# Performance work log

Hardware: AMD Instinct MI355X
Metric: run time of the kernel (lower is better)

The kernel has to match this reference:

```python
import jax, jax.numpy as jnp
import numpy as np

N, E, D, G, L = 100000, 1600000, 64, 512, 3
EPS = 1e-5


def setup_inputs() -> dict:
    key = jax.random.key(0)
    ks = jax.random.split(key, 8)
    x = jax.random.normal(ks[0], (N, D), dtype=jnp.float32)
    edge_index = jax.random.randint(ks[1], (2, E), 0, N, dtype=jnp.int32)
    batch = jnp.sort(jax.random.randint(ks[2], (N,), 0, G, dtype=jnp.int32))
    s = 1.0 / np.sqrt(D)
    convW = jax.random.normal(ks[3], (L, D, D), dtype=jnp.float32) * s
    convB = jnp.zeros((L, D), jnp.float32)
    bn_g = jnp.ones((L, D), jnp.float32); bn_b = jnp.zeros((L, D), jnp.float32)
    ln_g = jnp.ones((L, D), jnp.float32); ln_b = jnp.zeros((L, D), jnp.float32)
    W1 = jax.random.normal(ks[4], (3 * D, 2 * D), dtype=jnp.float32) * (1.0 / np.sqrt(3 * D))
    b1 = jnp.zeros((2 * D,), jnp.float32)
    ln1_g = jnp.ones((2 * D,), jnp.float32); ln1_b = jnp.zeros((2 * D,), jnp.float32)
    W2 = jax.random.normal(ks[5], (2 * D, D), dtype=jnp.float32) * (1.0 / np.sqrt(2 * D))
    b2 = jnp.zeros((D,), jnp.float32)
    ln2_g = jnp.ones((D,), jnp.float32); ln2_b = jnp.zeros((D,), jnp.float32)
    W3 = jax.random.normal(ks[6], (D, 1), dtype=jnp.float32) * s
    b3 = jnp.zeros((1,), jnp.float32)
    return dict(x=x, edge_index=edge_index, batch=batch, convW=convW, convB=convB,
                bn_g=bn_g, bn_b=bn_b, ln_g=ln_g, ln_b=ln_b,
                W1=W1, b1=b1, ln1_g=ln1_g, ln1_b=ln1_b,
                W2=W2, b2=b2, ln2_g=ln2_g, ln2_b=ln2_b, W3=W3, b3=b3)


def _layer_norm(h, g, b):
    mu = jnp.mean(h, axis=-1, keepdims=True)
    var = jnp.mean((h - mu) ** 2, axis=-1, keepdims=True)
    return (h - mu) * jax.lax.rsqrt(var + EPS) * g + b


def _forward(x, edge_index, batch, convW, convB, bn_g, bn_b, ln_g, ln_b,
             W1, b1, ln1_g, ln1_b, W2, b2, ln2_g, ln2_b, W3, b3):
    n = x.shape[0]
    loops = jnp.arange(n, dtype=edge_index.dtype)
    src = jnp.concatenate([edge_index[0], loops])  # self-loops as in GCNConv
    dst = jnp.concatenate([edge_index[1], loops])
    deg = jax.ops.segment_sum(jnp.ones_like(src, dtype=x.dtype), dst, num_segments=n)
    dinv = jnp.where(deg > 0, jax.lax.rsqrt(deg), 0.0)
    norm = (dinv[src] * dinv[dst])[:, None]  # [E+N, 1]

    h = x
    for i in range(L):
        x_in = h
        hw = h @ convW[i]                                   # [N, D]
        agg = jax.ops.segment_sum(norm * hw[src], dst, num_segments=n) + convB[i]
        # BatchNorm1d (train-mode batch stats, biased var)
        mu = jnp.mean(agg, axis=0)
        var = jnp.mean((agg - mu) ** 2, axis=0)
        hb = (agg - mu) * jax.lax.rsqrt(var + EPS) * bn_g[i] + bn_b[i]
        if i > 0:
            hb = hb + x_in  # residual (shapes match: D == D)
        h = jax.nn.gelu(_layer_norm(hb, ln_g[i], ln_b[i]), approximate=False)

    # multi-pool over graphs
    cnt = jax.ops.segment_sum(jnp.ones((n,), x.dtype), batch, num_segments=G)[:, None]
    s = jax.ops.segment_sum(h, batch, num_segments=G)
    mean = s / jnp.maximum(cnt, 1.0)
    mx = jax.ops.segment_max(h, batch, num_segments=G)
    mx = jnp.where(cnt > 0, mx, 0.0)
    z = jnp.concatenate([mean, mx, s], axis=1)  # [G, 3D]

    z = jax.nn.gelu(_layer_norm(z @ W1 + b1, ln1_g, ln1_b), approximate=False)
    z = jax.nn.gelu(_layer_norm(z @ W2 + b2, ln2_g, ln2_b), approximate=False)
    return z @ W3 + b3  # [G, num_classes]


def reference(x, edge_index, batch, convW, convB, bn_g, bn_b, ln_g, ln_b,
              W1, b1, ln1_g, ln1_b, W2, b2, ln2_g, ln2_b, W3, b3):
    return _forward(x, edge_index, batch, convW, convB, bn_g, bn_b, ln_g, ln_b,
                    W1, b1, ln1_g, ln1_b, W2, b2, ln2_g, ln2_b, W3, b3)
```

## Files before the change

### kernel.cpp

```cpp
#include <hip/hip_runtime.h>
#include <hip/hip_bf16.h>
#include <hip/hip_fp16.h>

#define DD 64
#define EPSV 1e-5f
#define NSLICE 16

typedef __attribute__((ext_vector_type(4))) _Float16 f16x4;
typedef __attribute__((ext_vector_type(8))) _Float16 f16x8;
typedef __attribute__((ext_vector_type(4))) float f32x4;

static __device__ __forceinline__ float fatomic_add(float* p, float v) {
#if defined(__HIP_DEVICE_COMPILE__)
    return unsafeAtomicAdd(p, v);
#else
    return 0.f;
#endif
}

static __device__ __forceinline__ float gelu_exact(float x) {
    return 0.5f * x * (1.0f + erff(x * 0.70710678118654752f));
}

static __device__ __forceinline__ void acc_u4(float* a8, uint4 v) {
    const __half2* hp = reinterpret_cast<const __half2*>(&v);
#pragma unroll
    for (int p = 0; p < 4; ++p) {
        float2 f = __half22float2(hp[p]);
        a8[2 * p] += f.x;
        a8[2 * p + 1] += f.y;
    }
}

#define ACHUNK 2048
#define NBMAX 400

__global__ __launch_bounds__(1024) void k_bcount(const int* __restrict__ dst,
                                                 int* __restrict__ bucketCnt,
                                                 int e, int nbuck) {
    __shared__ int h[NBMAX];
    int t = threadIdx.x;
    for (int i = t; i < nbuck; i += 1024) h[i] = 0;
    __syncthreads();
    int base = blockIdx.x * 8192;
#pragma unroll
    for (int k = 0; k < 8; ++k) {
        int i = base + k * 1024 + t;
        if (i < e) atomicAdd(&h[dst[i] >> 8], 1);
    }
    __syncthreads();
    for (int i = t; i < nbuck; i += 1024)
        if (h[i]) atomicAdd(&bucketCnt[i], h[i]);
}

__global__ __launch_bounds__(512) void k_bscan2(const int* __restrict__ bucketCnt,
                                                int* __restrict__ bbase,
                                                int* __restrict__ bcur,
                                                int* __restrict__ offs,
                                                int nbuck, int etotal, int n) {
    __shared__ int ws[8];
    int t = threadIdx.x, lane = t & 63, wv = t >> 6;
    int v = (t < nbuck) ? bucketCnt[t] : 0;
    int x = v;
#pragma unroll
    for (int o = 1; o < 64; o <<= 1) {
        int u = __shfl_up(x, o, 64);
        if (lane >= o) x += u;
    }
    if (lane == 63) ws[wv] = x;
    __syncthreads();
    int add = 0;
    for (int w = 0; w < wv; ++w) add += ws[w];
    int excl = add + x - v;
    if (t < nbuck) {
        bbase[t] = excl;
        bcur[t] = excl;
    }
    if (t == 0) {
        bbase[nbuck] = etotal;
        offs[n] = etotal;
    }
}

__global__ __launch_bounds__(1024) void k_dhist(const int* __restrict__ off,
                                                int* __restrict__ dcount, int n) {
    __shared__ int h[256];
    int t = threadIdx.x;
    if (t < 256) h[t] = 0;
    __syncthreads();
    int i = blockIdx.x * 1024 + t;
    if (i < n) {
        int d = min(off[i + 1] - off[i], 255);
        atomicAdd(&h[d], 1);
    }
    __syncthreads();
    if (t < 256 && h[t]) atomicAdd(&dcount[t], h[t]);
}

__global__ __launch_bounds__(256) void k_dscan(const int* __restrict__ dcount,
                                               int* __restrict__ dcur) {
    __shared__ int ws[4];
    int t = threadIdx.x;
    int lane = t & 63, wv = t >> 6;
    int v = dcount[t];
    int x = v;
#pragma unroll
    for (int o = 1; o < 64; o <<= 1) {
        int u = __shfl_up(x, o, 64);
        if (lane >= o) x += u;
    }
    if (lane == 63) ws[wv] = x;
    __syncthreads();
    int add = 0;
    for (int w = 0; w < wv; ++w) add += ws[w];
    dcur[t] = add + x - v;
}

__global__ __launch_bounds__(1024) void k_dscatter(const int* __restrict__ off,
                                                   int* __restrict__ dcur,
                                                   int* __restrict__ perm, int n) {
    __shared__ int lcnt[256], lbase[256];
    int t = threadIdx.x;
    if (t < 256) lcnt[t] = 0;
    __syncthreads();
    int i = blockIdx.x * 1024 + t;
    int d = 0, rank = 0;
    if (i < n) {
        d = min(off[i + 1] - off[i], 255);
        rank = atomicAdd(&lcnt[d], 1);
    }
    __syncthreads();
    if (t < 256 && lcnt[t]) lbase[t] = atomicAdd(&dcur[t], lcnt[t]);
    __syncthreads();
    if (i < n) perm[lbase[d] + rank] = i;
}

__global__ __launch_bounds__(256) void k_binA(const int* __restrict__ src,
                                              const int* __restrict__ dst,
                                              int* __restrict__ ebuf,
                                              int* __restrict__ bcur,
                                              int e, int nbuck) {
    __shared__ int cnt[NBMAX], startb[NBMAX], posb[NBMAX], gbase[NBMAX];
    __shared__ int stage[ACHUNK];
    __shared__ unsigned short stb[ACHUNK];
    int t = threadIdx.x;
    for (int cbase = blockIdx.x * ACHUNK; cbase < e; cbase += gridDim.x * ACHUNK) {
        int cval = min(ACHUNK, e - cbase);
        for (int i = t; i < nbuck; i += 256) { cnt[i] = 0; posb[i] = 0; }
        __syncthreads();
        int eb[8], es[8];
#pragma unroll
        for (int k = 0; k < 8; ++k) {
            int i = t + k * 256;
            if (i < cval) {
                int s = src[cbase + i];
                int d = dst[cbase + i];
                eb[k] = d >> 8;
                es[k] = s | ((d & 255) << 24);
                atomicAdd(&cnt[eb[k]], 1);
            } else eb[k] = -1;
        }
        __syncthreads();
        if (t == 0) {
            int r = 0;
            for (int b2 = 0; b2 < nbuck; ++b2) { startb[b2] = r; r += cnt[b2]; }
        }
        __syncthreads();
        for (int i = t; i < nbuck; i += 256)
            if (cnt[i] > 0) gbase[i] = atomicAdd(&bcur[i], cnt[i]);
#pragma unroll
        for (int k = 0; k < 8; ++k)
            if (eb[k] >= 0) {
                int idx = startb[eb[k]] + atomicAdd(&posb[eb[k]], 1);
                stage[idx] = es[k];
                stb[idx] = (unsigned short)eb[k];
            }
        __syncthreads();
        for (int i = t; i < cval; i += 256) {
            int b2 = stb[i];
            ebuf[gbase[b2] + (i - startb[b2])] = stage[i];
        }
        __syncthreads();
    }
}

__global__ __launch_bounds__(256) void k_binB(const int* __restrict__ ebuf,
                                              const int* __restrict__ bbase,
                                              int* __restrict__ offs,
                                              float* __restrict__ dinv,
                                              int* __restrict__ csr, int n) {
    __shared__ int cnt[256], cur[256], ws[4];
    int b = blockIdx.x;
    int base = b << 8;
    int nn = min(256, n - base);
    int t = threadIdx.x;
    int e0 = bbase[b], e1 = bbase[b + 1];
    cnt[t] = 0;
    __syncthreads();
    for (int i = e0 + t; i < e1; i += 256)
        atomicAdd(&cnt[((unsigned)ebuf[i]) >> 24], 1);
    __syncthreads();
    int v = cnt[t];
    int lane = t & 63, wv = t >> 6;
    int x = v;
#pragma unroll
    for (int o = 1; o < 64; o <<= 1) {
        int u = __shfl_up(x, o, 64);
        if (lane >= o) x += u;
    }
    if (lane == 63) ws[wv] = x;
    __syncthreads();
    int add = 0;
    for (int w = 0; w < wv; ++w) add += ws[w];
    int excl = add + x - v;
    if (t < nn) {
        offs[base + t] = e0 + excl;
        dinv[base + t] = rsqrtf((float)v + 1.0f);
    }
    cur[t] = e0 + excl;
    __syncthreads();
    for (int i = e0 + t; i < e1; i += 256) {
        int packed = ebuf[i];
        int dl = ((unsigned)packed) >> 24;
        int pos = atomicAdd(&cur[dl], 1);
        csr[pos] = packed & 0x00FFFFFF;
    }
}

__global__ void k_misc(const float* __restrict__ x, const float* __restrict__ dinv,
                       __half* __restrict__ mA, __half* __restrict__ mB, int n,
                       const int* __restrict__ batch, int* __restrict__ bnd, int g) {
    int i = blockIdx.x * 256 + threadIdx.x;
    int total = n * 64;
    if (i < total) {
        mA[i] = __float2half_rn(x[i] * dinv[i >> 6]);
    } else if (i < total + 64) {
        mA[i] = __float2half_rn(0.f);
        mB[i] = __float2half_rn(0.f);
    }
    if (i < n) {
        int b = batch[i];
        if (i == 0)
            for (int q = 0; q <= b; ++q) bnd[q] = 0;
        else {
            int pb = batch[i - 1];
            for (int q = pb + 1; q <= b; ++q) bnd[q] = i;
        }
        if (i == n - 1)
            for (int q = b + 1; q <= g; ++q) bnd[q] = n;
    }
}

__global__ __launch_bounds__(256, 4) void k_gather_gemm(const int* __restrict__ off,
                                                        const int* __restrict__ csr,
                                                        const float* __restrict__ dinv,
                                                        const __half* __restrict__ m16,
                                                        const float* __restrict__ W,
                                                        const float* __restrict__ convB,
                                                        const int* __restrict__ perm,
                                                        float* __restrict__ agg,
                                                        float* __restrict__ gstat,
                                                        int n, int nzero) {
    __shared__ float sred[128];
    const int t = threadIdx.x;
    const int lane = t & 63, wv = t >> 6;
    const int g = lane >> 4, ln = lane & 15;

    f16x8 bfr[2][4];
#pragma unroll
    for (int kt = 0; kt < 2; ++kt)
#pragma unroll
        for (int nt = 0; nt < 4; ++nt) {
            f16x8 h;
#pragma unroll
            for (int j = 0; j < 8; ++j)
                h[j] = (_Float16)W[(32 * kt + 8 * g + j) * 64 + 16 * nt + ln];
            bfr[kt][nt] = h;
        }

    if (t < 128) sred[t] = 0.f;
    __syncthreads();

    const int ntiles = (n + 15) >> 4;
    const int tile = blockIdx.x * 4 + wv;
    float s_acc[4] = {0.f, 0.f, 0.f, 0.f}, q_acc[4] = {0.f, 0.f, 0.f, 0.f};

    if (tile < ntiles) {
        const int slot = tile * 16 + ln;
        const bool valid = slot < n;
        const int node = valid ? perm[slot] : -1;
        const int row_self = valid ? node : nzero;
        int a = 0, deg = 0;
        float dd = 0.f;
        if (valid) {
            a = off[node];
            deg = off[node + 1] - a;
            dd = dinv[node];
        }
        int md = deg;
#pragma unroll
        for (int o = 1; o < 64; o <<= 1) md = max(md, __shfl_xor(md, o, 64));

        float acc[2][8];
#pragma unroll
        for (int kt = 0; kt < 2; ++kt)
#pragma unroll
            for (int j = 0; j < 8; ++j) acc[kt][j] = 0.f;

        const uint4* mrow4 = (const uint4*)m16;
        {
            const uint4* rp = mrow4 + ((size_t)row_self << 3) + g;
            uint4 v0 = rp[0], v1 = rp[4];
            acc_u4(acc[0], v0);
            acc_u4(acc[1], v1);
        }
        int ecur[4];
#pragma unroll
        for (int k = 0; k < 4; ++k) ecur[k] = (k < deg) ? csr[a + k] : nzero;
        for (int i = 0; i < md; i += 4) {
            int enx[4];
#pragma unroll
            for (int k = 0; k < 4; ++k) enx[k] = (i + 4 + k < deg) ? csr[a + i + 4 + k] : nzero;
            uint4 v[4][2];
#pragma unroll
            for (int r = 0; r < 4; ++r) {
                const uint4* rp = mrow4 + ((size_t)ecur[r] << 3) + g;
                v[r][0] = rp[0];
                v[r][1] = rp[4];
            }
#pragma unroll
            for (int r = 0; r < 4; ++r) {
                acc_u4(acc[0], v[r][0]);
                acc_u4(acc[1], v[r][1]);
            }
#pragma unroll
            for (int k = 0; k < 4; ++k) ecur[k] = enx[k];
        }

        f32x4 c[4];
#pragma unroll
        for (int nt = 0; nt < 4; ++nt) c[nt] = (f32x4){0.f, 0.f, 0.f, 0.f};
#pragma unroll
        for (int kt = 0; kt < 2; ++kt) {
            f16x8 ah, ar;
#pragma unroll
            for (int j = 0; j < 8; ++j) {
                float v = acc[kt][j] * dd;
                _Float16 h = (_Float16)v;
                ah[j] = h;
                ar[j] = (_Float16)(v - (float)h);
            }
#pragma unroll
            for (int nt = 0; nt < 4; ++nt) {
                c[nt] = __builtin_amdgcn_mfma_f32_16x16x32_f16(ah, bfr[kt][nt], c[nt], 0, 0, 0);
                c[nt] = __builtin_amdgcn_mfma_f32_16x16x32_f16(ar, bfr[kt][nt], c[nt], 0, 0, 0);
            }
        }

        int prow[4];
#pragma unroll
        for (int i = 0; i < 4; ++i) prow[i] = __shfl(node, 4 * g + i, 64);
        const float bias[4] = {convB[ln], convB[16 + ln], convB[32 + ln], convB[48 + ln]};
#pragma unroll
        for (int nt = 0; nt < 4; ++nt) {
#pragma unroll
            for (int i = 0; i < 4; ++i) {
                if (prow[i] >= 0) {
                    float v = c[nt][i] + bias[nt];
                    agg[(size_t)prow[i] * 64 + 16 * nt + ln] = v;
                    s_acc[nt] += v;
                    q_acc[nt] += v * v;
                }
            }
        }
#pragma unroll
        for (int nt = 0; nt < 4; ++nt) {
            s_acc[nt] += __shfl_xor(s_acc[nt], 16, 64);
            s_acc[nt] += __shfl_xor(s_acc[nt], 32, 64);
            q_acc[nt] += __shfl_xor(q_acc[nt], 16, 64);
            q_acc[nt] += __shfl_xor(q_acc[nt], 32, 64);
        }
        if (g == 0) {
#pragma unroll
            for (int nt = 0; nt < 4; ++nt) {
                atomicAdd(&sred[16 * nt + ln], s_acc[nt]);
                atomicAdd(&sred[64 + 16 * nt + ln], q_acc[nt]);
            }
        }
    }
    __syncthreads();
    if (t < 64) {
        float* gs = gstat + (blockIdx.x & (NSLICE - 1)) * 128;
        fatomic_add(&gs[t], sred[t]);
        fatomic_add(&gs[64 + t], sred[64 + t]);
    }
}

__global__ __launch_bounds__(256) void k_bn_ln_gelu(const float* __restrict__ agg,
                                                    const __half* __restrict__ m16res,
                                                    const float* __restrict__ gstat,
                                                    const float* __restrict__ dinv,
                                                    const float* __restrict__ bng,
                                                    const float* __restrict__ bnb,
                                                    const float* __restrict__ lng,
                                                    const float* __restrict__ lnb,
                                                    __half* __restrict__ m16out,
                                                    int n, int has_res, int scale_out) {
    int t = threadIdx.x;
    int lane = t & 63, wv = t >> 6;
    float fs = 0.f, fq = 0.f;
#pragma unroll
    for (int s = 0; s < NSLICE; ++s) {
        fs += gstat[s * 128 + lane];
        fq += gstat[s * 128 + 64 + lane];
    }
    float invN = 1.0f / (float)n;
    float mu_c = fs * invN;
    float var_c = fq * invN - mu_c * mu_c;
    float bscale = rsqrtf(var_c + EPSV) * bng[lane];
    float bshift = bnb[lane];
    float lg = lng[lane], lb = lnb[lane];
    for (int r = blockIdx.x * 4 + wv; r < n; r += gridDim.x * 4) {
        float dd = dinv[r];
        float x = agg[(size_t)r * 64 + lane];
        float hb = (x - mu_c) * bscale + bshift;
        if (has_res) hb += __half2float(m16res[(size_t)r * 64 + lane]) * (1.0f / dd);
        float ssum = hb;
#pragma unroll
        for (int off = 32; off; off >>= 1) ssum += __shfl_xor(ssum, off, 64);
        float rmu = ssum * (1.f / 64.f);
        float d = hb - rmu;
        float vs = d * d;
#pragma unroll
        for (int off = 32; off; off >>= 1) vs += __shfl_xor(vs, off, 64);
        float rvar = vs * (1.f / 64.f);
        float ln = d * rsqrtf(rvar + EPSV) * lg + lb;
        float g = gelu_exact(ln);
        float outv = scale_out ? g * dd : g;
        m16out[(size_t)r * 64 + lane] = __float2half_rn(outv);
    }
}

__global__ __launch_bounds__(256) void k_pool_z(const __half* __restrict__ h,
                                                const int* __restrict__ bnd,
                                                float* __restrict__ z) {
    int g = blockIdx.x;
    int t = threadIdx.x;
    int lane = t & 63, wv = t >> 6;
    int s0 = bnd[g], e0 = bnd[g + 1];
    float s = 0.f, mx = -INFINITY;
    for (int i = s0 + wv; i < e0; i += 4) {
        float v = __half2float(h[(size_t)i * 64 + lane]);
        s += v;
        mx = fmaxf(mx, v);
    }
    __shared__ float ss[256], sm[256];
    ss[t] = s;
    sm[t] = mx;
    __syncthreads();
    if (t < 64) {
        float fs = ss[t] + ss[t + 64] + ss[t + 128] + ss[t + 192];
        float fm = fmaxf(fmaxf(sm[t], sm[t + 64]), fmaxf(sm[t + 128], sm[t + 192]));
        float cntf = (float)(e0 - s0);
        float mean = fs / fmaxf(cntf, 1.0f);
        if (e0 == s0) fm = 0.f;
        z[g * 192 + t] = mean;
        z[g * 192 + 64 + t] = fm;
        z[g * 192 + 128 + t] = fs;
    }
}

__global__ __launch_bounds__(128) void k_head(const float* __restrict__ z,
                                              const float* __restrict__ W1, const float* __restrict__ b1,
                                              const float* __restrict__ ln1g, const float* __restrict__ ln1b,
                                              const float* __restrict__ W2, const float* __restrict__ b2,
                                              const float* __restrict__ ln2g, const float* __restrict__ ln2b,
                                              const float* __restrict__ W3, const float* __restrict__ b3,
                                              float* __restrict__ out) {
    int g = blockIdx.x;
    int t = threadIdx.x;
    int lane = t & 63, wv = t >> 6;
    __shared__ float zl[192], h1[128], red[2];
    for (int i = t; i < 192; i += 128) zl[i] = z[g * 192 + i];
    __syncthreads();
    float acc = b1[t];
    for (int k = 0; k < 192; ++k) acc += zl[k] * W1[k * 128 + t];
    float s = acc;
#pragma unroll
    for (int off = 32; off; off >>= 1) s += __shfl_xor(s, off, 64);
    if (lane == 0) red[wv] = s;
    __syncthreads();
    float mu = (red[0] + red[1]) * (1.f / 128.f);
    float d = acc - mu;
    float q = d * d;
#pragma unroll
    for (int off = 32; off; off >>= 1) q += __shfl_xor(q, off, 64);
    __syncthreads();
    if (lane == 0) red[wv] = q;
    __syncthreads();
    float var = (red[0] + red[1]) * (1.f / 128.f);
    float ln = d * rsqrtf(var + EPSV) * ln1g[t] + ln1b[t];
    h1[t] = gelu_exact(ln);
    __syncthreads();
    if (t < 64) {
        float acc2 = b2[t];
        for (int k = 0; k < 128; ++k) acc2 += h1[k] * W2[k * 64 + t];
        float s2 = acc2;
#pragma unroll
        for (int off = 32; off; off >>= 1) s2 += __shfl_xor(s2, off, 64);
        float mu2 = s2 * (1.f / 64.f);
        float d2 = acc2 - mu2;
        float q2 = d2 * d2;
#pragma unroll
        for (int off = 32; off; off >>= 1) q2 += __shfl_xor(q2, off, 64);
        float var2 = q2 * (1.f / 64.f);
        float l2 = d2 * rsqrtf(var2 + EPSV) * ln2g[t] + ln2b[t];
        float g2 = gelu_exact(l2);
        float p = g2 * W3[t];
#pragma unroll
        for (int off = 32; off; off >>= 1) p += __shfl_xor(p, off, 64);
        if (t == 0) out[g] = p + b3[0];
    }
}

extern "C" void kernel_launch(void* const* d_in, const int* in_sizes, int n_in,
                              void* d_out, int out_size, void* d_ws, size_t ws_size,
                              hipStream_t stream) {
    const float* x      = (const float*)d_in[0];
    const int*   eidx   = (const int*)d_in[1];
    const int*   batch  = (const int*)d_in[2];
    const float* convW  = (const float*)d_in[3];
    const float* convB  = (const float*)d_in[4];
    const float* bn_g   = (const float*)d_in[5];
    const float* bn_b   = (const float*)d_in[6];
    const float* ln_g   = (const float*)d_in[7];
    const float* ln_b   = (const float*)d_in[8];
    const float* W1     = (const float*)d_in[9];
    const float* b1     = (const float*)d_in[10];
    const float* ln1g   = (const float*)d_in[11];
    const float* ln1b   = (const float*)d_in[12];
    const float* W2     = (const float*)d_in[13];
    const float* b2     = (const float*)d_in[14];
    const float* ln2g   = (const float*)d_in[15];
    const float* ln2b   = (const float*)d_in[16];
    const float* W3     = (const float*)d_in[17];
    const float* b3     = (const float*)d_in[18];
    float* out = (float*)d_out;

    const int N = in_sizes[0] / DD;
    const int E = in_sizes[1] / 2;
    const int G = out_size;
    const int* esrc = eidx;
    const int* edst = eidx + E;

    char* ws = (char*)d_ws;
    size_t off_b = 0;
    auto alloc = [&](size_t bytes) {
        size_t p = off_b;
        off_b = (off_b + bytes + 255) & ~(size_t)255;
        return (void*)(ws + p);
    };
    int*    offs   = (int*)alloc((size_t)(N + 1) * 4);
    float*  dinv   = (float*)alloc((size_t)N * 4);
    int*    csr    = (int*)alloc((size_t)E * 4);
    int*    ebuf   = (int*)alloc((size_t)E * 4);
    __half* m16A   = (__half*)alloc((size_t)(N + 1) * DD * 2);
    __half* m16B   = (__half*)alloc((size_t)(N + 1) * DD * 2);
    float*  aggbuf = (float*)alloc((size_t)N * DD * 4);
    float*  gstats = (float*)alloc((size_t)3 * NSLICE * 128 * 4);
    int*    perm   = (int*)alloc((size_t)N * 4);
    int*    dcount = (int*)alloc(256 * 4);
    int*    dcur   = (int*)alloc(256 * 4);
    int*    bnd    = (int*)alloc((size_t)(G + 1) * 4);
    int*    bucketCnt = (int*)alloc((size_t)NBMAX * 4);
    int*    bbase  = (int*)alloc((size_t)(NBMAX + 1) * 4);
    int*    bcur   = (int*)alloc(((size_t)(N + 255) / 256) * 4);
    float* z = aggbuf;
    (void)ws_size; (void)n_in;

    const int nbuck = (N + 255) / 256;
    const int nb = (N + 1023) / 1024;

    hipMemsetAsync(gstats, 0, (size_t)3 * NSLICE * 128 * 4, stream);
    hipMemsetAsync(dcount, 0, 256 * 4, stream);
    hipMemsetAsync(bucketCnt, 0, (size_t)NBMAX * 4, stream);
    k_bcount<<<(E + 8191) / 8192, 1024, 0, stream>>>(edst, bucketCnt, E, nbuck);
    k_bscan2<<<1, 512, 0, stream>>>(bucketCnt, bbase, bcur, offs, nbuck, E, N);
    k_binA<<<(E + ACHUNK - 1) / ACHUNK, 256, 0, stream>>>(esrc, edst, ebuf, bcur, E, nbuck);
    k_binB<<<nbuck, 256, 0, stream>>>(ebuf, bbase, offs, dinv, csr, N);
    k_dhist<<<nb, 1024, 0, stream>>>(offs, dcount, N);
    k_dscan<<<1, 256, 0, stream>>>(dcount, dcur);
    k_dscatter<<<nb, 1024, 0, stream>>>(offs, dcur, perm, N);
    k_misc<<<((N + 1) * DD + 255) / 256, 256, 0, stream>>>(x, dinv, m16A, m16B, N, batch, bnd, G);

    __half* gin[3]  = {m16A, m16B, m16A};
    __half* gout[3] = {m16B, m16A, m16B};

    const int ntiles = (N + 15) / 16;
    const int gblocks = (ntiles + 3) / 4;

    for (int l = 0; l < 3; ++l) {
        float* gstat = gstats + (size_t)l * NSLICE * 128;
        k_gather_gemm<<<gblocks, 256, 0, stream>>>(offs, csr, dinv, (const __half*)gin[l],
                                                   convW + (size_t)l * DD * DD, convB + l * DD,
                                                   perm, aggbuf, gstat, N, N);
        k_bn_ln_gelu<<<2048, 256, 0, stream>>>(aggbuf, gin[l], gstat, dinv,
                                               bn_g + l * DD, bn_b + l * DD,
                                               ln_g + l * DD, ln_b + l * DD,
                                               gout[l], N, l > 0 ? 1 : 0, l < 2 ? 1 : 0);
    }

    k_pool_z<<<G, 256, 0, stream>>>(m16B, bnd, z);
    k_head<<<G, 128, 0, stream>>>(z, W1, b1, ln1g, ln1b, W2, b2, ln2g, ln2b, W3, b3, out);
}
```

Before: 418.6 us.

## Fuse prep kernels, precompute slot info, store aggregates in fp16, merge pool and head

Several independent changes. The x*dinv fp16 conversion moves into k_binB and the batch boundary setup into k_dhist, which removes k_misc. A k_slotinfo pass packs per-slot offset, degree, node and dinv into int4 so the gather kernel needs one load instead of chained perm/off/dinv loads. The aggregate buffer becomes fp16, halving its write and read traffic between the GEMM and BN kernels at some precision cost. Pooling and the MLP head are fused into one kernel, and the three memsets are merged into one.

```diff
diff --git a/kernel.cpp b/kernel.cpp
--- a/kernel.cpp
+++ b/kernel.cpp
@@ -83,7 +83,12 @@
 }
 
 __global__ __launch_bounds__(1024) void k_dhist(const int* __restrict__ off,
-                                                int* __restrict__ dcount, int n) {
+                                                int* __restrict__ dcount,
+                                                const int* __restrict__ batch,
+                                                int* __restrict__ bnd,
+                                                __half* __restrict__ mA,
+                                                __half* __restrict__ mB,
+                                                int n, int g) {
     __shared__ int h[256];
     int t = threadIdx.x;
     if (t < 256) h[t] = 0;
@@ -92,6 +97,19 @@
     if (i < n) {
         int d = min(off[i + 1] - off[i], 255);
         atomicAdd(&h[d], 1);
+        int b = batch[i];
+        if (i == 0)
+            for (int q = 0; q <= b; ++q) bnd[q] = 0;
+        else {
+            int pb = batch[i - 1];
+            for (int q = pb + 1; q <= b; ++q) bnd[q] = i;
+        }
+        if (i == n - 1)
+            for (int q = b + 1; q <= g; ++q) bnd[q] = n;
+    }
+    if (blockIdx.x == 0 && t < 64) {
+        mA[(size_t)n * 64 + t] = __float2half_rn(0.f);
+        mB[(size_t)n * 64 + t] = __float2half_rn(0.f);
     }
     __syncthreads();
     if (t < 256 && h[t]) atomicAdd(&dcount[t], h[t]);
@@ -133,6 +151,22 @@
     if (t < 256 && lcnt[t]) lbase[t] = atomicAdd(&dcur[t], lcnt[t]);
     __syncthreads();
     if (i < n) perm[lbase[d] + rank] = i;
+}
+
+__global__ __launch_bounds__(1024) void k_slotinfo(const int* __restrict__ off,
+                                                   const float* __restrict__ dinv,
+                                                   const int* __restrict__ perm,
+                                                   int4* __restrict__ sinfo,
+                                                   int n, int ntiles) {
+    int s = blockIdx.x * 1024 + threadIdx.x;
+    if (s < n) {
+        int node = perm[s];
+        int a = off[node];
+        int d = off[node + 1] - a;
+        sinfo[s] = make_int4(a, d, node, __float_as_int(dinv[node]));
+    } else if (s < ntiles * 16) {
+        sinfo[s] = make_int4(0, 0, -1, 0);
+    }
 }
 
 __global__ __launch_bounds__(256) void k_binA(const int* __restrict__ src,
@@ -186,10 +220,13 @@
 
 __global__ __launch_bounds__(256) void k_binB(const int* __restrict__ ebuf,
                                               const int* __restrict__ bbase,
+                                              const float* __restrict__ x,
                                               int* __restrict__ offs,
                                               float* __restrict__ dinv,
+                                              __half* __restrict__ mA,
                                               int* __restrict__ csr, int n) {
     __shared__ int cnt[256], cur[256], ws[4];
+    __shared__ float sdinv[256];
     int b = blockIdx.x;
     int base = b << 8;
     int nn = min(256, n - base);
@@ -202,23 +239,31 @@
     __syncthreads();
     int v = cnt[t];
     int lane = t & 63, wv = t >> 6;
-    int x = v;
+    int x2 = v;
 #pragma unroll
     for (int o = 1; o < 64; o <<= 1) {
-        int u = __shfl_up(x, o, 64);
-        if (lane >= o) x += u;
-    }
-    if (lane == 63) ws[wv] = x;
+        int u = __shfl_up(x2, o, 64);
+        if (lane >= o) x2 += u;
+    }
+    if (lane == 63) ws[wv] = x2;
     __syncthreads();
     int add = 0;
     for (int w = 0; w < wv; ++w) add += ws[w];
-    int excl = add + x - v;
+    int excl = add + x2 - v;
+    float dv = rsqrtf((float)v + 1.0f);
     if (t < nn) {
         offs[base + t] = e0 + excl;
-        dinv[base + t] = rsqrtf((float)v + 1.0f);
-    }
+        dinv[base + t] = dv;
+    }
+    sdinv[t] = dv;
     cur[t] = e0 + excl;
     __syncthreads();
+    const int tot = nn * 64;
+    const size_t gbase2 = (size_t)base * 64;
+    for (int i = t; i < tot; i += 256) {
+        float val = x[gbase2 + i] * sdinv[i >> 6];
+        mA[gbase2 + i] = __float2half_rn(val);
+    }
     for (int i = e0 + t; i < e1; i += 256) {
         int packed = ebuf[i];
         int dl = ((unsigned)packed) >> 24;
@@ -227,38 +272,12 @@
     }
 }
 
-__global__ void k_misc(const float* __restrict__ x, const float* __restrict__ dinv,
-                       __half* __restrict__ mA, __half* __restrict__ mB, int n,
-                       const int* __restrict__ batch, int* __restrict__ bnd, int g) {
-    int i = blockIdx.x * 256 + threadIdx.x;
-    int total = n * 64;
-    if (i < total) {
-        mA[i] = __float2half_rn(x[i] * dinv[i >> 6]);
-    } else if (i < total + 64) {
-        mA[i] = __float2half_rn(0.f);
-        mB[i] = __float2half_rn(0.f);
-    }
-    if (i < n) {
-        int b = batch[i];
-        if (i == 0)
-            for (int q = 0; q <= b; ++q) bnd[q] = 0;
-        else {
-            int pb = batch[i - 1];
-            for (int q = pb + 1; q <= b; ++q) bnd[q] = i;
-        }
-        if (i == n - 1)
-            for (int q = b + 1; q <= g; ++q) bnd[q] = n;
-    }
-}
-
-__global__ __launch_bounds__(256, 4) void k_gather_gemm(const int* __restrict__ off,
+__global__ __launch_bounds__(256, 4) void k_gather_gemm(const int4* __restrict__ sinfo,
                                                         const int* __restrict__ csr,
-                                                        const float* __restrict__ dinv,
                                                         const __half* __restrict__ m16,
                                                         const float* __restrict__ W,
                                                         const float* __restrict__ convB,
-                                                        const int* __restrict__ perm,
-                                                        float* __restrict__ agg,
+                                                        __half* __restrict__ agg,
                                                         float* __restrict__ gstat,
                                                         int n, int nzero) {
     __shared__ float sred[128];
@@ -277,6 +296,7 @@
                 h[j] = (_Float16)W[(32 * kt + 8 * g + j) * 64 + 16 * nt + ln];
             bfr[kt][nt] = h;
         }
+    const float bias[4] = {convB[ln], convB[16 + ln], convB[32 + ln], convB[48 + ln]};
 
     if (t < 128) sred[t] = 0.f;
     __syncthreads();
@@ -284,19 +304,14 @@
     const int ntiles = (n + 15) >> 4;
     const int tile = blockIdx.x * 4 + wv;
     float s_acc[4] = {0.f, 0.f, 0.f, 0.f}, q_acc[4] = {0.f, 0.f, 0.f, 0.f};
+    const uint4* mrow4 = (const uint4*)m16;
 
     if (tile < ntiles) {
-        const int slot = tile * 16 + ln;
-        const bool valid = slot < n;
-        const int node = valid ? perm[slot] : -1;
-        const int row_self = valid ? node : nzero;
-        int a = 0, deg = 0;
-        float dd = 0.f;
-        if (valid) {
-            a = off[node];
-            deg = off[node + 1] - a;
-            dd = dinv[node];
-        }
+        const int4 si = sinfo[tile * 16 + ln];
+        const int a = si.x, deg = si.y, node = si.z;
+        const float dd = __int_as_float(si.w);
+        const int row_self = (node >= 0) ? node : nzero;
+
         int md = deg;
 #pragma unroll
         for (int o = 1; o < 64; o <<= 1) md = max(md, __shfl_xor(md, o, 64));
@@ -307,7 +322,6 @@
 #pragma unroll
             for (int j = 0; j < 8; ++j) acc[kt][j] = 0.f;
 
-        const uint4* mrow4 = (const uint4*)m16;
         {
             const uint4* rp = mrow4 + ((size_t)row_self << 3) + g;
             uint4 v0 = rp[0], v1 = rp[4];
@@ -360,32 +374,32 @@
         int prow[4];
 #pragma unroll
         for (int i = 0; i < 4; ++i) prow[i] = __shfl(node, 4 * g + i, 64);
-        const float bias[4] = {convB[ln], convB[16 + ln], convB[32 + ln], convB[48 + ln]};
 #pragma unroll
         for (int nt = 0; nt < 4; ++nt) {
 #pragma unroll
             for (int i = 0; i < 4; ++i) {
                 if (prow[i] >= 0) {
                     float v = c[nt][i] + bias[nt];
-                    agg[(size_t)prow[i] * 64 + 16 * nt + ln] = v;
+                    agg[(size_t)prow[i] * 64 + 16 * nt + ln] = __float2half_rn(v);
                     s_acc[nt] += v;
                     q_acc[nt] += v * v;
                 }
             }
         }
+    }
+
+#pragma unroll
+    for (int nt = 0; nt < 4; ++nt) {
+        s_acc[nt] += __shfl_xor(s_acc[nt], 16, 64);
+        s_acc[nt] += __shfl_xor(s_acc[nt], 32, 64);
+        q_acc[nt] += __shfl_xor(q_acc[nt], 16, 64);
+        q_acc[nt] += __shfl_xor(q_acc[nt], 32, 64);
+    }
+    if (g == 0) {
 #pragma unroll
         for (int nt = 0; nt < 4; ++nt) {
-            s_acc[nt] += __shfl_xor(s_acc[nt], 16, 64);
-            s_acc[nt] += __shfl_xor(s_acc[nt], 32, 64);
-            q_acc[nt] += __shfl_xor(q_acc[nt], 16, 64);
-            q_acc[nt] += __shfl_xor(q_acc[nt], 32, 64);
-        }
-        if (g == 0) {
-#pragma unroll
-            for (int nt = 0; nt < 4; ++nt) {
-                atomicAdd(&sred[16 * nt + ln], s_acc[nt]);
-                atomicAdd(&sred[64 + 16 * nt + ln], q_acc[nt]);
-            }
+            atomicAdd(&sred[16 * nt + ln], s_acc[nt]);
+            atomicAdd(&sred[64 + 16 * nt + ln], q_acc[nt]);
         }
     }
     __syncthreads();
@@ -396,7 +410,7 @@
     }
 }
 
-__global__ __launch_bounds__(256) void k_bn_ln_gelu(const float* __restrict__ agg,
+__global__ __launch_bounds__(256) void k_bn_ln_gelu(const __half* __restrict__ agg,
                                                     const __half* __restrict__ m16res,
                                                     const float* __restrict__ gstat,
                                                     const float* __restrict__ dinv,
@@ -422,7 +436,7 @@
     float lg = lng[lane], lb = lnb[lane];
     for (int r = blockIdx.x * 4 + wv; r < n; r += gridDim.x * 4) {
         float dd = dinv[r];
-        float x = agg[(size_t)r * 64 + lane];
+        float x = __half2float(agg[(size_t)r * 64 + lane]);
         float hb = (x - mu_c) * bscale + bshift;
         if (has_res) hb += __half2float(m16res[(size_t)r * 64 + lane]) * (1.0f / dd);
         float ssum = hb;
@@ -441,12 +455,18 @@
     }
 }
 
-__global__ __launch_bounds__(256) void k_pool_z(const __half* __restrict__ h,
-                                                const int* __restrict__ bnd,
-                                                float* __restrict__ z) {
+__global__ __launch_bounds__(256) void k_poolhead(const __half* __restrict__ h,
+                                                  const int* __restrict__ bnd,
+                                                  const float* __restrict__ W1, const float* __restrict__ b1,
+                                                  const float* __restrict__ ln1g, const float* __restrict__ ln1b,
+                                                  const float* __restrict__ W2, const float* __restrict__ b2,
+                                                  const float* __restrict__ ln2g, const float* __restrict__ ln2b,
+                                                  const float* __restrict__ W3, const float* __restrict__ b3,
+                                                  float* __restrict__ out) {
     int g = blockIdx.x;
     int t = threadIdx.x;
     int lane = t & 63, wv = t >> 6;
+    __shared__ float ss[256], sm[256], zl[192], h1[128], red[2];
     int s0 = bnd[g], e0 = bnd[g + 1];
     float s = 0.f, mx = -INFINITY;
     for (int i = s0 + wv; i < e0; i += 4) {
@@ -454,7 +474,6 @@
         s += v;
         mx = fmaxf(mx, v);
     }
-    __shared__ float ss[256], sm[256];
     ss[t] = s;
     sm[t] = mx;
     __syncthreads();
@@ -464,31 +483,20 @@
         float cntf = (float)(e0 - s0);
         float mean = fs / fmaxf(cntf, 1.0f);
         if (e0 == s0) fm = 0.f;
-        z[g * 192 + t] = mean;
-        z[g * 192 + 64 + t] = fm;
-        z[g * 192 + 128 + t] = fs;
-    }
-}
-
-__global__ __launch_bounds__(128) void k_head(const float* __restrict__ z,
-                                              const float* __restrict__ W1, const float* __restrict__ b1,
-                                              const float* __restrict__ ln1g, const float* __restrict__ ln1b,
-                                              const float* __restrict__ W2, const float* __restrict__ b2,
-                                              const float* __restrict__ ln2g, const float* __restrict__ ln2b,
-                                              const float* __restrict__ W3, const float* __restrict__ b3,
-                                              float* __restrict__ out) {
-    int g = blockIdx.x;
-    int t = threadIdx.x;
-    int lane = t & 63, wv = t >> 6;
-    __shared__ float zl[192], h1[128], red[2];
-    for (int i = t; i < 192; i += 128) zl[i] = z[g * 192 + i];
-    __syncthreads();
-    float acc = b1[t];
-    for (int k = 0; k < 192; ++k) acc += zl[k] * W1[k * 128 + t];
-    float s = acc;
-#pragma unroll
-    for (int off = 32; off; off >>= 1) s += __shfl_xor(s, off, 64);
-    if (lane == 0) red[wv] = s;
+        zl[t] = mean;
+        zl[64 + t] = fm;
+        zl[128 + t] = fs;
+    }
+    __syncthreads();
+    float acc = 0.f;
+    if (t < 128) {
+        acc = b1[t];
+        for (int k = 0; k < 192; ++k) acc += zl[k] * W1[k * 128 + t];
+    }
+    float s1 = acc;
+#pragma unroll
+    for (int off = 32; off; off >>= 1) s1 += __shfl_xor(s1, off, 64);
+    if (lane == 0 && wv < 2) red[wv] = s1;
     __syncthreads();
     float mu = (red[0] + red[1]) * (1.f / 128.f);
     float d = acc - mu;
@@ -496,11 +504,13 @@
 #pragma unroll
     for (int off = 32; off; off >>= 1) q += __shfl_xor(q, off, 64);
     __syncthreads();
-    if (lane == 0) red[wv] = q;
+    if (lane == 0 && wv < 2) red[wv] = q;
     __syncthreads();
     float var = (red[0] + red[1]) * (1.f / 128.f);
-    float ln = d * rsqrtf(var + EPSV) * ln1g[t] + ln1b[t];
-    h1[t] = gelu_exact(ln);
+    if (t < 128) {
+        float ln = d * rsqrtf(var + EPSV) * ln1g[t] + ln1b[t];
+        h1[t] = gelu_exact(ln);
+    }
     __syncthreads();
     if (t < 64) {
         float acc2 = b2[t];
@@ -560,56 +570,55 @@
         off_b = (off_b + bytes + 255) & ~(size_t)255;
         return (void*)(ws + p);
     };
+    const int ntiles = (N + 15) / 16;
+    const int gblocks = (ntiles + 3) / 4;
+
+    float*  gstats = (float*)alloc((size_t)3 * NSLICE * 128 * 4);
+    int*    dcount = (int*)alloc(256 * 4);
+    int*    bucketCnt = (int*)alloc((size_t)NBMAX * 4);
+    const size_t zero_bytes = 3 * NSLICE * 128 * 4 + 1024 + 1792;
     int*    offs   = (int*)alloc((size_t)(N + 1) * 4);
     float*  dinv   = (float*)alloc((size_t)N * 4);
     int*    csr    = (int*)alloc((size_t)E * 4);
     int*    ebuf   = (int*)alloc((size_t)E * 4);
     __half* m16A   = (__half*)alloc((size_t)(N + 1) * DD * 2);
     __half* m16B   = (__half*)alloc((size_t)(N + 1) * DD * 2);
-    float*  aggbuf = (float*)alloc((size_t)N * DD * 4);
-    float*  gstats = (float*)alloc((size_t)3 * NSLICE * 128 * 4);
+    __half* aggbuf = (__half*)alloc((size_t)N * DD * 2);
     int*    perm   = (int*)alloc((size_t)N * 4);
-    int*    dcount = (int*)alloc(256 * 4);
+    int4*   sinfo  = (int4*)alloc((size_t)ntiles * 16 * 16);
     int*    dcur   = (int*)alloc(256 * 4);
     int*    bnd    = (int*)alloc((size_t)(G + 1) * 4);
-    int*    bucketCnt = (int*)alloc((size_t)NBMAX * 4);
     int*    bbase  = (int*)alloc((size_t)(NBMAX + 1) * 4);
     int*    bcur   = (int*)alloc(((size_t)(N + 255) / 256) * 4);
-    float* z = aggbuf;
     (void)ws_size; (void)n_in;
 
     const int nbuck = (N + 255) / 256;
     const int nb = (N + 1023) / 1024;
 
-    hipMemsetAsync(gstats, 0, (size_t)3 * NSLICE * 128 * 4, stream);
-    hipMemsetAsync(dcount, 0, 256 * 4, stream);
-    hipMemsetAsync(bucketCnt, 0, (size_t)NBMAX * 4, stream);
+    hipMemsetAsync(gstats, 0, zero_bytes, stream);
     k_bcount<<<(E + 8191) / 8192, 1024, 0, stream>>>(edst, bucketCnt, E, nbuck);
     k_bscan2<<<1, 512, 0, stream>>>(bucketCnt, bbase, bcur, offs, nbuck, E, N);
     k_binA<<<(E + ACHUNK - 1) / ACHUNK, 256, 0, stream>>>(esrc, edst, ebuf, bcur, E, nbuck);
-    k_binB<<<nbuck, 256, 0, stream>>>(ebuf, bbase, offs, dinv, csr, N);
-    k_dhist<<<nb, 1024, 0, stream>>>(offs, dcount, N);
+    k_binB<<<nbuck, 256, 0, stream>>>(ebuf, bbase, x, offs, dinv, m16A, csr, N);
+    k_dhist<<<nb, 1024, 0, stream>>>(offs, dcount, batch, bnd, m16A, m16B, N, G);
     k_dscan<<<1, 256, 0, stream>>>(dcount, dcur);
     k_dscatter<<<nb, 1024, 0, stream>>>(offs, dcur, perm, N);
-    k_misc<<<((N + 1) * DD + 255) / 256, 256, 0, stream>>>(x, dinv, m16A, m16B, N, batch, bnd, G);
+    k_slotinfo<<<(ntiles * 16 + 1023) / 1024, 1024, 0, stream>>>(offs, dinv, perm, sinfo, N, ntiles);
 
     __half* gin[3]  = {m16A, m16B, m16A};
     __half* gout[3] = {m16B, m16A, m16B};
 
-    const int ntiles = (N + 15) / 16;
-    const int gblocks = (ntiles + 3) / 4;
-
     for (int l = 0; l < 3; ++l) {
         float* gstat = gstats + (size_t)l * NSLICE * 128;
-        k_gather_gemm<<<gblocks, 256, 0, stream>>>(offs, csr, dinv, (const __half*)gin[l],
+        k_gather_gemm<<<gblocks, 256, 0, stream>>>(sinfo, csr, (const __half*)gin[l],
                                                    convW + (size_t)l * DD * DD, convB + l * DD,
-                                                   perm, aggbuf, gstat, N, N);
+                                                   aggbuf, gstat, N, N);
         k_bn_ln_gelu<<<2048, 256, 0, stream>>>(aggbuf, gin[l], gstat, dinv,
                                                bn_g + l * DD, bn_b + l * DD,
                                                ln_g + l * DD, ln_b + l * DD,
                                                gout[l], N, l > 0 ? 1 : 0, l < 2 ? 1 : 0);
     }
 
-    k_pool_z<<<G, 256, 0, stream>>>(m16B, bnd, z);
-    k_head<<<G, 128, 0, stream>>>(z, W1, b1, ln1g, ln1b, W2, b2, ln2g, ln2b, W3, b3, out);
-}
+    k_poolhead<<<G, 256, 0, stream>>>(m16B, bnd, W1, b1, ln1g, ln1b,
+                                      W2, b2, ln2g, ln2b, W3, b3, out);
+}
```

After: 402.5 us. -3.9%, faster.
